# Kernel optimization log

Measured on AMD Instinct MI355X. Metric: run time of the kernel, lower is better.

## Reference

```python
import jax, jax.numpy as jnp
import numpy as np

IN_NC = 512

def setup_inputs() -> dict:
    key = jax.random.key(0)
    k1, k2, k3, k4 = jax.random.split(key, 4)
    B, N = 8, 2048
    nd, out_nc = 512, 512
    x = jax.random.normal(k1, (B, N * IN_NC), dtype=jnp.float32)
    # store weights as [in_nc, d] so projection is x @ W (same math as torch Linear with W^T)
    Wq = jax.random.normal(k2, (IN_NC, nd), dtype=jnp.float32) * (1.0 / np.sqrt(IN_NC))
    Wk = jax.random.normal(k3, (IN_NC, nd), dtype=jnp.float32) * (1.0 / np.sqrt(IN_NC))
    Wv = jax.random.normal(k4, (IN_NC, out_nc), dtype=jnp.float32) * (1.0 / np.sqrt(IN_NC))
    return {"x": x, "Wq": Wq, "Wk": Wk, "Wv": Wv}

def reference(x, Wq, Wk, Wv):
    B = x.shape[0]
    N = x.shape[1] // IN_NC
    xt = x.reshape(B, N, IN_NC)                     # [B, N, in_nc]
    Q = jnp.einsum('bnc,cd->bnd', xt, Wq)           # [B, N, nd]
    K = jnp.einsum('bnc,cd->bnd', xt, Wk)           # [B, N, nd]
    V = jnp.einsum('bnc,cd->bnd', xt, Wv)           # [B, N, out_nc]
    A = jnp.einsum('bnd,bmd->bnm', Q, K)            # [B, N, N]  (no scale, as in source)
    A = jax.nn.softmax(A, axis=-1)
    out = jnp.einsum('bnm,bmd->bnd', A, V)          # [B, N, out_nc]
    return out.reshape(B, -1)
```

## Files before the change

kernel.cpp:

```cpp
#include <hip/hip_runtime.h>
#include <hip/hip_fp16.h>

typedef _Float16 f16x8 __attribute__((ext_vector_type(8)));
typedef _Float16 f16x4 __attribute__((ext_vector_type(4)));
typedef float    f32x4 __attribute__((ext_vector_type(4)));

#define LOG2E 1.44269504f

__device__ __forceinline__ void stage128x64(const _Float16* __restrict__ g, int ld,
                                            void* lds, int tid)
{
    const int r0   = tid >> 3;
    const int colh = ((tid & 7) ^ (r0 & 7)) << 3;
    char* lbase = (char*)lds + (tid >> 6) * 1024;
#pragma unroll
    for (int i = 0; i < 4; i++) {
        const _Float16* src = g + (size_t)(i * 32 + r0) * ld + colh;
        __builtin_amdgcn_global_load_lds(
            (const __attribute__((address_space(1))) void*)src,
            (__attribute__((address_space(3))) void*)(lbase + i * 4096),
            16, 0, 0);
    }
}

__device__ __forceinline__ f16x8 lds_frag(const void* lds, int row, int colh)
{
    const int off = row * 128 + ((colh * 2) ^ ((row & 7) << 4));
    return *(const f16x8*)((const char*)lds + off);
}

template<int NK>
__device__ __forceinline__ void gemm_loop_cv(const _Float16* __restrict__ A, int lda,
                                             const _Float16* __restrict__ B, int ldb,
                                             _Float16* a0, _Float16* a1,
                                             _Float16* b0, _Float16* b1,
                                             f32x4 acc[4][4], int tid,
                                             int wr, int wc, int lrow, int lkg)
{
    stage128x64(A, lda, a0, tid);
    stage128x64(B, ldb, b0, tid);
    stage128x64(A + 64, lda, a1, tid);
    stage128x64(B + 64, ldb, b1, tid);
    asm volatile("s_waitcnt vmcnt(8)" ::: "memory");
    __builtin_amdgcn_s_barrier();
    __builtin_amdgcn_sched_barrier(0);

    for (int t = 0; t < NK; ++t) {
        _Float16* acur = (t & 1) ? a1 : a0;
        _Float16* bcur = (t & 1) ? b1 : b0;

        f16x8 af[2][4], bf[2][4];
#pragma unroll
        for (int kk = 0; kk < 2; kk++) {
#pragma unroll
            for (int mi = 0; mi < 4; mi++)
                af[kk][mi] = lds_frag(acur, wr * 64 + mi * 16 + lrow, kk * 32 + lkg * 8);
#pragma unroll
            for (int ni = 0; ni < 4; ni++)
                bf[kk][ni] = lds_frag(bcur, wc * 64 + ni * 16 + lrow, kk * 32 + lkg * 8);
        }
        asm volatile("s_waitcnt lgkmcnt(0)" ::: "memory");
        __builtin_amdgcn_sched_barrier(0);
        __builtin_amdgcn_s_barrier();

        if (t + 2 < NK) {
            stage128x64(A + (size_t)(t + 2) * 64, lda, acur, tid);
            stage128x64(B + (size_t)(t + 2) * 64, ldb, bcur, tid);
        }
        __builtin_amdgcn_sched_barrier(0);

        __builtin_amdgcn_s_setprio(1);
#pragma unroll
        for (int kk = 0; kk < 2; kk++)
#pragma unroll
            for (int mi = 0; mi < 4; mi++)
#pragma unroll
                for (int ni = 0; ni < 4; ni++)
                    acc[mi][ni] = __builtin_amdgcn_mfma_f32_16x16x32_f16(
                        af[kk][mi], bf[kk][ni], acc[mi][ni], 0, 0, 0);
        __builtin_amdgcn_s_setprio(0);

        if (t + 2 < NK) asm volatile("s_waitcnt vmcnt(8)" ::: "memory");
        else            asm volatile("s_waitcnt vmcnt(0)" ::: "memory");
        __builtin_amdgcn_sched_barrier(0);
        __builtin_amdgcn_s_barrier();
        __builtin_amdgcn_sched_barrier(0);
    }
}

__global__ __launch_bounds__(256)
void convert_kernel(const float* __restrict__ x,
                    const float* __restrict__ Wq,
                    const float* __restrict__ Wk,
                    const float* __restrict__ Wv,
                    _Float16* __restrict__ xh,
                    _Float16* __restrict__ Wt)
{
    const int b = blockIdx.x;
    if (b < 2048) {
        const size_t base = (size_t)b * 4096 + (size_t)threadIdx.x * 4;
#pragma unroll
        for (int i = 0; i < 4; i++) {
            f32x4 v = *(const f32x4*)(x + base + i * 1024);
            f16x4 h;
#pragma unroll
            for (int j = 0; j < 4; j++) h[j] = (_Float16)v[j];
            *(f16x4*)(xh + base + i * 1024) = h;
        }
    } else {
        __shared__ float tb[32][33];
        const int t = b - 2048;
        const int mat = t >> 8;
        const int tile = t & 255;
        const int tr = tile >> 4, tc = tile & 15;
        const float* W = (mat == 0) ? Wq : (mat == 1) ? Wk : Wv;
        const int r = threadIdx.x >> 5, c = threadIdx.x & 31;
#pragma unroll
        for (int p = 0; p < 4; p++)
            tb[p * 8 + r][c] = W[(size_t)(tr * 32 + p * 8 + r) * 512 + tc * 32 + c];
        __syncthreads();
#pragma unroll
        for (int p = 0; p < 4; p++)
            Wt[((size_t)mat * 512 + tc * 32 + p * 8 + r) * 512 + tr * 32 + c] =
                (_Float16)tb[c][p * 8 + r];
    }
}

__global__ __launch_bounds__(256, 2)
void proj_kernel(const _Float16* __restrict__ xh,
                 const _Float16* __restrict__ Wt,
                 _Float16* __restrict__ Qf,
                 _Float16* __restrict__ Kf,
                 _Float16* __restrict__ Vt)
{
    __shared__ _Float16 a0[128 * 64], a1[128 * 64];
    __shared__ _Float16 b0[128 * 64], b1[128 * 64];

    const int tid = threadIdx.x;
    const int mb = blockIdx.x, cb = blockIdx.y;
    const int mat = cb >> 2, nb = cb & 3;
    const int m0 = mb * 128, n0 = nb * 128;

    const _Float16* Abase = xh + (size_t)m0 * 512;
    const _Float16* Bbase = Wt + ((size_t)mat * 512 + n0) * 512;

    const int lane = tid & 63;
    const int w = tid >> 6;
    const int wr = w >> 1, wc = w & 1;
    const int lrow = lane & 15, lkg = lane >> 4;

    f32x4 acc[4][4];
#pragma unroll
    for (int i = 0; i < 4; i++)
#pragma unroll
        for (int j = 0; j < 4; j++) acc[i][j] = (f32x4)0.0f;

    gemm_loop_cv<8>(Abase, 512, Bbase, 512, a0, a1, b0, b1,
                    acc, tid, wr, wc, lrow, lkg);

    if (mat < 2) {
        _Float16* Out = (mat == 0) ? Qf : Kf;
#pragma unroll
        for (int mi = 0; mi < 4; mi++) {
            const int mbase = m0 + wr * 64 + mi * 16 + lkg * 4;
#pragma unroll
            for (int ni = 0; ni < 4; ni++) {
                const int ncol = n0 + wc * 64 + ni * 16 + lrow;
#pragma unroll
                for (int r = 0; r < 4; r++)
                    Out[(size_t)(mbase + r) * 512 + ncol] = (_Float16)acc[mi][ni][r];
            }
        }
    } else {
#pragma unroll
        for (int mi = 0; mi < 4; mi++) {
            const int mglob = m0 + wr * 64 + mi * 16 + lkg * 4;
            const int b = mglob >> 11, mloc = mglob & 2047;
#pragma unroll
            for (int ni = 0; ni < 4; ni++) {
                const int d = n0 + wc * 64 + ni * 16 + lrow;
                f16x4 h;
#pragma unroll
                for (int r = 0; r < 4; r++) h[r] = (_Float16)acc[mi][ni][r];
                *(f16x4*)&Vt[((size_t)b * 512 + d) * 2048 + mloc] = h;
            }
        }
    }
}

__global__ __launch_bounds__(256, 2)
void score_kernel(const _Float16* __restrict__ Qf,
                  const _Float16* __restrict__ Kf,
                  _Float16* __restrict__ P,
                  float2* __restrict__ ML, int b0)
{
    __shared__ __align__(16) char smem[65536];
    _Float16* a0  = (_Float16*)smem;
    _Float16* a1  = (_Float16*)(smem + 16384);
    _Float16* b0p = (_Float16*)(smem + 32768);
    _Float16* b1p = (_Float16*)(smem + 49152);
    float (*S_lds)[132] = (float(*)[132])smem;

    const int tid = threadIdx.x;
    const int mb = blockIdx.x, nb = blockIdx.y, bl = blockIdx.z;
    const int bg = b0 + bl;

    const _Float16* Abase = Qf + (size_t)(bg * 2048 + nb * 128) * 512;
    const _Float16* Bbase = Kf + (size_t)(bg * 2048 + mb * 128) * 512;

    const int lane = tid & 63;
    const int w = tid >> 6;
    const int wr = w >> 1, wc = w & 1;
    const int lrow = lane & 15, lkg = lane >> 4;

    f32x4 acc[4][4];
#pragma unroll
    for (int i = 0; i < 4; i++)
#pragma unroll
        for (int j = 0; j < 4; j++) acc[i][j] = (f32x4)0.0f;

    gemm_loop_cv<8>(Abase, 512, Bbase, 512, a0, a1, b0p, b1p,
                    acc, tid, wr, wc, lrow, lkg);

    _Float16* Pb = P + (size_t)bl * 2048 * 2048;
    const int s  = tid >> 2;
    const int q4 = tid & 3;

#pragma unroll
    for (int hp = 0; hp < 2; hp++) {
#pragma unroll
        for (int m2 = 0; m2 < 2; m2++) {
            const int mi = hp * 2 + m2;
            const int srow = wr * 32 + m2 * 16 + lkg * 4;
#pragma unroll
            for (int ni = 0; ni < 4; ni++) {
                const int col = wc * 64 + ni * 16 + lrow;
#pragma unroll
                for (int rr = 0; rr < 4; rr++)
                    S_lds[srow + rr][col] = acc[mi][ni][rr];
            }
        }
        __syncthreads();

        f32x4 vv[8];
#pragma unroll
        for (int seg = 0; seg < 4; seg++) {
            vv[seg * 2 + 0] = *(const f32x4*)&S_lds[s][q4 * 8 + seg * 32 + 0];
            vv[seg * 2 + 1] = *(const f32x4*)&S_lds[s][q4 * 8 + seg * 32 + 4];
        }

        float m = vv[0][0];
#pragma unroll
        for (int j = 0; j < 8; j++)
#pragma unroll
            for (int jj = 0; jj < 4; jj++) m = fmaxf(m, vv[j][jj]);
        m = fmaxf(m, __shfl_xor(m, 1));
        m = fmaxf(m, __shfl_xor(m, 2));

        float l = 0.0f;
#pragma unroll
        for (int j = 0; j < 8; j++)
#pragma unroll
            for (int jj = 0; jj < 4; jj++) {
                float e = exp2f((vv[j][jj] - m) * LOG2E);
                vv[j][jj] = e;
                l += e;
            }
        l += __shfl_xor(l, 1);
        l += __shfl_xor(l, 2);

        const int q_local = (s >> 5) * 64 + hp * 32 + (s & 31);
        const int q = nb * 128 + q_local;

        if (q4 == 0) {
            float2 v; v.x = m; v.y = l;
            ML[((size_t)bl * 2048 + q) * 16 + mb] = v;
        }

#pragma unroll
        for (int seg = 0; seg < 4; seg++) {
            f16x8 h;
#pragma unroll
            for (int jj = 0; jj < 4; jj++) {
                h[jj]     = (_Float16)vv[seg * 2 + 0][jj];
                h[jj + 4] = (_Float16)vv[seg * 2 + 1][jj];
            }
            *(f16x8*)&Pb[(size_t)q * 2048 + mb * 128 + q4 * 8 + seg * 32] = h;
        }
        __syncthreads();
    }
}

__global__ __launch_bounds__(256, 2)
void out_kernel(const _Float16* __restrict__ P,
                const _Float16* __restrict__ Vt,
                const float2* __restrict__ ML,
                float* __restrict__ out, int b0)
{
    __shared__ _Float16 a0[128 * 64], a1[128 * 64];
    __shared__ _Float16 b0p[128 * 64], b1p[128 * 64];
    __shared__ float scale_lds[128][17];

    const int tid = threadIdx.x;
    const int db = blockIdx.x >> 4, nb = blockIdx.x & 15, bl = blockIdx.y;
    const int bg = b0 + bl;

    if (tid < 128) {
        const float2* mlrow = ML + ((size_t)bl * 2048 + nb * 128 + tid) * 16;
        float2 ml[16];
        float M = -3.4e38f;
#pragma unroll
        for (int t = 0; t < 16; t++) { ml[t] = mlrow[t]; M = fmaxf(M, ml[t].x); }
        float L = 0.0f;
#pragma unroll
        for (int t = 0; t < 16; t++) L += ml[t].y * exp2f((ml[t].x - M) * LOG2E);
        const float invL = 1.0f / L;
#pragma unroll
        for (int t = 0; t < 16; t++)
            scale_lds[tid][t] = exp2f((ml[t].x - M) * LOG2E) * invL;
    }

    const _Float16* Abase = P  + (size_t)bl * 2048 * 2048 + (size_t)(nb * 128) * 2048;
    const _Float16* Bbase = Vt + (size_t)bg * 512  * 2048 + (size_t)(db * 128) * 2048;

    const int lane = tid & 63;
    const int w = tid >> 6;
    const int wr = w >> 1, wc = w & 1;
    const int lrow = lane & 15, lkg = lane >> 4;

    f32x4 acc[4][4];
#pragma unroll
    for (int i = 0; i < 4; i++)
#pragma unroll
        for (int j = 0; j < 4; j++) acc[i][j] = (f32x4)0.0f;

    __syncthreads();

    stage128x64(Abase,      2048, a0,  tid);
    stage128x64(Bbase,      2048, b0p, tid);
    stage128x64(Abase + 64, 2048, a1,  tid);
    stage128x64(Bbase + 64, 2048, b1p, tid);
    asm volatile("s_waitcnt vmcnt(8)" ::: "memory");
    __builtin_amdgcn_s_barrier();
    __builtin_amdgcn_sched_barrier(0);

    for (int t = 0; t < 32; ++t) {
        _Float16* acur = (t & 1) ? a1 : a0;
        _Float16* bcur = (t & 1) ? b1p : b0p;
        const int kt = t >> 1;

        f16x8 af[2][4], bf[2][4];
        float sc[4];
#pragma unroll
        for (int kk = 0; kk < 2; kk++) {
#pragma unroll
            for (int mi = 0; mi < 4; mi++)
                af[kk][mi] = lds_frag(acur, wr * 64 + mi * 16 + lrow, kk * 32 + lkg * 8);
#pragma unroll
            for (int ni = 0; ni < 4; ni++)
                bf[kk][ni] = lds_frag(bcur, wc * 64 + ni * 16 + lrow, kk * 32 + lkg * 8);
        }
#pragma unroll
        for (int mi = 0; mi < 4; mi++)
            sc[mi] = scale_lds[wr * 64 + mi * 16 + lrow][kt];
        asm volatile("s_waitcnt lgkmcnt(0)" ::: "memory");
        __builtin_amdgcn_sched_barrier(0);
        __builtin_amdgcn_s_barrier();

        if (t + 2 < 32) {
            stage128x64(Abase + (size_t)(t + 2) * 64, 2048, acur, tid);
            stage128x64(Bbase + (size_t)(t + 2) * 64, 2048, bcur, tid);
        }
        __builtin_amdgcn_sched_barrier(0);

        __builtin_amdgcn_s_setprio(1);
#pragma unroll
        for (int kk = 0; kk < 2; kk++)
#pragma unroll
            for (int mi = 0; mi < 4; mi++) {
                const f16x8 a = af[kk][mi] * (_Float16)sc[mi];
#pragma unroll
                for (int ni = 0; ni < 4; ni++)
                    acc[mi][ni] = __builtin_amdgcn_mfma_f32_16x16x32_f16(
                        a, bf[kk][ni], acc[mi][ni], 0, 0, 0);
            }
        __builtin_amdgcn_s_setprio(0);

        if (t + 2 < 32) asm volatile("s_waitcnt vmcnt(8)" ::: "memory");
        else            asm volatile("s_waitcnt vmcnt(0)" ::: "memory");
        __builtin_amdgcn_sched_barrier(0);
        __builtin_amdgcn_s_barrier();
        __builtin_amdgcn_sched_barrier(0);
    }

#pragma unroll
    for (int mi = 0; mi < 4; mi++) {
        const int nbase = nb * 128 + wr * 64 + mi * 16 + lkg * 4;
#pragma unroll
        for (int ni = 0; ni < 4; ni++) {
            const int d = db * 128 + wc * 64 + ni * 16 + lrow;
#pragma unroll
            for (int rr = 0; rr < 4; rr++)
                out[((size_t)bg * 2048 + nbase + rr) * 512 + d] = acc[mi][ni][rr];
        }
    }
}

extern "C" void kernel_launch(void* const* d_in, const int* in_sizes, int n_in,
                              void* d_out, int out_size, void* d_ws, size_t ws_size,
                              hipStream_t stream) {
    const float* x  = (const float*)d_in[0];
    const float* Wq = (const float*)d_in[1];
    const float* Wk = (const float*)d_in[2];
    const float* Wv = (const float*)d_in[3];

    const size_t MB = 1024ull * 1024ull;
    char* ws = (char*)d_ws;
    _Float16* Qf = (_Float16*)ws;
    _Float16* Kf = Qf + (size_t)16384 * 512;
    _Float16* Vt = Kf + (size_t)16384 * 512;
    _Float16* P  = Vt + (size_t)16384 * 512;
    float*    out = (float*)d_out;

    int chunk;
    if      (ws_size >= 120 * MB) chunk = 8;
    else if (ws_size >= 88  * MB) chunk = 4;
    else if (ws_size >= 70  * MB) chunk = 2;
    else                          chunk = 1;

    float2* ML = (float2*)(P + (size_t)chunk * 2048 * 2048);

    _Float16* xh = (_Float16*)P;
    _Float16* Wt = xh + (size_t)16384 * 512;

    convert_kernel<<<2816, 256, 0, stream>>>(x, Wq, Wk, Wv, xh, Wt);
    proj_kernel<<<dim3(128, 12), 256, 0, stream>>>(xh, Wt, Qf, Kf, Vt);

    for (int b0 = 0; b0 < 8; b0 += chunk) {
        score_kernel<<<dim3(16, 16, chunk), 256, 0, stream>>>(Qf, Kf, P, ML, b0);
        out_kernel<<<dim3(64, chunk), 256, 0, stream>>>(P, Vt, ML, out, b0);
    }
}
```

Before: 135.9 us.

## Compute transposed score tile to do softmax reductions in registers

```diff
diff --git a/kernel.cpp b/kernel.cpp
--- a/kernel.cpp
+++ b/kernel.cpp
@@ -199,14 +199,15 @@
     _Float16* a1  = (_Float16*)(smem + 16384);
     _Float16* b0p = (_Float16*)(smem + 32768);
     _Float16* b1p = (_Float16*)(smem + 49152);
-    float (*S_lds)[132] = (float(*)[132])smem;
+    float (*redm)[128] = (float(*)[128])smem;
+    float (*reds)[128] = (float(*)[128])(smem + 1024);
 
     const int tid = threadIdx.x;
     const int mb = blockIdx.x, nb = blockIdx.y, bl = blockIdx.z;
     const int bg = b0 + bl;
 
-    const _Float16* Abase = Qf + (size_t)(bg * 2048 + nb * 128) * 512;
-    const _Float16* Bbase = Kf + (size_t)(bg * 2048 + mb * 128) * 512;
+    const _Float16* Abase = Kf + (size_t)(bg * 2048 + mb * 128) * 512;
+    const _Float16* Bbase = Qf + (size_t)(bg * 2048 + nb * 128) * 512;
 
     const int lane = tid & 63;
     const int w = tid >> 6;
@@ -223,71 +224,74 @@
                     acc, tid, wr, wc, lrow, lkg);
 
     _Float16* Pb = P + (size_t)bl * 2048 * 2048;
-    const int s  = tid >> 2;
-    const int q4 = tid & 3;
-
-#pragma unroll
-    for (int hp = 0; hp < 2; hp++) {
-#pragma unroll
-        for (int m2 = 0; m2 < 2; m2++) {
-            const int mi = hp * 2 + m2;
-            const int srow = wr * 32 + m2 * 16 + lkg * 4;
-#pragma unroll
-            for (int ni = 0; ni < 4; ni++) {
-                const int col = wc * 64 + ni * 16 + lrow;
-#pragma unroll
-                for (int rr = 0; rr < 4; rr++)
-                    S_lds[srow + rr][col] = acc[mi][ni][rr];
-            }
-        }
-        __syncthreads();
-
-        f32x4 vv[8];
-#pragma unroll
-        for (int seg = 0; seg < 4; seg++) {
-            vv[seg * 2 + 0] = *(const f32x4*)&S_lds[s][q4 * 8 + seg * 32 + 0];
-            vv[seg * 2 + 1] = *(const f32x4*)&S_lds[s][q4 * 8 + seg * 32 + 4];
-        }
-
-        float m = vv[0][0];
-#pragma unroll
-        for (int j = 0; j < 8; j++)
-#pragma unroll
-            for (int jj = 0; jj < 4; jj++) m = fmaxf(m, vv[j][jj]);
-        m = fmaxf(m, __shfl_xor(m, 1));
-        m = fmaxf(m, __shfl_xor(m, 2));
-
+
+    float mt[4], lt[4];
+#pragma unroll
+    for (int ni = 0; ni < 4; ni++) {
+        float m = acc[0][ni][0];
+#pragma unroll
+        for (int mi = 0; mi < 4; mi++)
+#pragma unroll
+            for (int rr = 0; rr < 4; rr++) m = fmaxf(m, acc[mi][ni][rr]);
+        m = fmaxf(m, __shfl_xor(m, 16));
+        m = fmaxf(m, __shfl_xor(m, 32));
+        mt[ni] = m;
+    }
+    if (lkg == 0) {
+#pragma unroll
+        for (int ni = 0; ni < 4; ni++)
+            redm[wr][wc * 64 + ni * 16 + lrow] = mt[ni];
+    }
+    __syncthreads();
+#pragma unroll
+    for (int ni = 0; ni < 4; ni++)
+        mt[ni] = fmaxf(mt[ni], redm[wr ^ 1][wc * 64 + ni * 16 + lrow]);
+
+#pragma unroll
+    for (int ni = 0; ni < 4; ni++) {
         float l = 0.0f;
 #pragma unroll
-        for (int j = 0; j < 8; j++)
-#pragma unroll
-            for (int jj = 0; jj < 4; jj++) {
-                float e = exp2f((vv[j][jj] - m) * LOG2E);
-                vv[j][jj] = e;
+        for (int mi = 0; mi < 4; mi++)
+#pragma unroll
+            for (int rr = 0; rr < 4; rr++) {
+                float e = exp2f((acc[mi][ni][rr] - mt[ni]) * LOG2E);
+                acc[mi][ni][rr] = e;
                 l += e;
             }
-        l += __shfl_xor(l, 1);
-        l += __shfl_xor(l, 2);
-
-        const int q_local = (s >> 5) * 64 + hp * 32 + (s & 31);
-        const int q = nb * 128 + q_local;
-
-        if (q4 == 0) {
-            float2 v; v.x = m; v.y = l;
+        l += __shfl_xor(l, 16);
+        l += __shfl_xor(l, 32);
+        lt[ni] = l;
+    }
+    if (lkg == 0) {
+#pragma unroll
+        for (int ni = 0; ni < 4; ni++)
+            reds[wr][wc * 64 + ni * 16 + lrow] = lt[ni];
+    }
+    __syncthreads();
+#pragma unroll
+    for (int ni = 0; ni < 4; ni++)
+        lt[ni] += reds[wr ^ 1][wc * 64 + ni * 16 + lrow];
+
+    if (wr == 0 && lkg == 0) {
+#pragma unroll
+        for (int ni = 0; ni < 4; ni++) {
+            const int q = nb * 128 + wc * 64 + ni * 16 + lrow;
+            float2 v; v.x = mt[ni]; v.y = lt[ni];
             ML[((size_t)bl * 2048 + q) * 16 + mb] = v;
         }
-
-#pragma unroll
-        for (int seg = 0; seg < 4; seg++) {
-            f16x8 h;
-#pragma unroll
-            for (int jj = 0; jj < 4; jj++) {
-                h[jj]     = (_Float16)vv[seg * 2 + 0][jj];
-                h[jj + 4] = (_Float16)vv[seg * 2 + 1][jj];
-            }
-            *(f16x8*)&Pb[(size_t)q * 2048 + mb * 128 + q4 * 8 + seg * 32] = h;
-        }
-        __syncthreads();
+    }
+
+#pragma unroll
+    for (int ni = 0; ni < 4; ni++) {
+        const int q = nb * 128 + wc * 64 + ni * 16 + lrow;
+        _Float16* prow = Pb + (size_t)q * 2048 + mb * 128 + wr * 64 + lkg * 4;
+#pragma unroll
+        for (int mi = 0; mi < 4; mi++) {
+            f16x4 h;
+#pragma unroll
+            for (int rr = 0; rr < 4; rr++) h[rr] = (_Float16)acc[mi][ni][rr];
+            *(f16x4*)&prow[mi * 16] = h;
+        }
     }
 }
 
```

Measured after the change: 143.4 us. 1.05x slower.
